# Kernel tuning notes

Measured on AMD Instinct MI355X. Metric: run time of the kernel, lower is better.

The kernel has to match this reference:

```python
import jax, jax.numpy as jnp
import numpy as np

NUM_NODES = 100000
NUM_EDGES = 1600000
NUM_GRAPHS = 512
HIDDEN = 128
LAYERS = 3
NUM_CLASSES = 10
BN_EPS = 1e-5


def setup_inputs() -> dict:
    key = jax.random.key(0)
    ks = jax.random.split(key, 12)
    x = jax.random.normal(ks[0], (NUM_NODES, HIDDEN), dtype=jnp.float32)
    edge_index = jax.random.randint(ks[1], (2, NUM_EDGES), 0, NUM_NODES, dtype=jnp.int32)
    batch = jnp.sort(jax.random.randint(ks[2], (NUM_NODES,), 0, NUM_GRAPHS, dtype=jnp.int32))
    s = 1.0 / np.sqrt(HIDDEN)
    W1 = jax.random.normal(ks[3], (LAYERS, HIDDEN, HIDDEN), dtype=jnp.float32) * s
    b1 = jnp.zeros((LAYERS, HIDDEN), dtype=jnp.float32)
    W2 = jax.random.normal(ks[4], (LAYERS, HIDDEN, HIDDEN), dtype=jnp.float32) * s
    b2 = jnp.zeros((LAYERS, HIDDEN), dtype=jnp.float32)
    gamma = jnp.ones((LAYERS, HIDDEN), dtype=jnp.float32)
    beta = jnp.zeros((LAYERS, HIDDEN), dtype=jnp.float32)
    eps_gin = jnp.zeros((LAYERS,), dtype=jnp.float32)  # train_eps init 0
    lin1_w = jax.random.normal(ks[5], (LAYERS * HIDDEN, HIDDEN), dtype=jnp.float32) * (1.0 / np.sqrt(LAYERS * HIDDEN))
    lin1_b = jnp.zeros((HIDDEN,), dtype=jnp.float32)
    lin2_w = jax.random.normal(ks[6], (HIDDEN, NUM_CLASSES), dtype=jnp.float32) * s
    lin2_b = jnp.zeros((NUM_CLASSES,), dtype=jnp.float32)
    return {"x": x, "edge_index": edge_index, "batch": batch,
            "W1": W1, "b1": b1, "W2": W2, "b2": b2,
            "gamma": gamma, "beta": beta, "eps_gin": eps_gin,
            "lin1_w": lin1_w, "lin1_b": lin1_b, "lin2_w": lin2_w, "lin2_b": lin2_b}


def _batchnorm(h, g, b):
    mu = jnp.mean(h, axis=0, keepdims=True)
    var = jnp.var(h, axis=0, keepdims=True)
    return (h - mu) * jax.lax.rsqrt(var + BN_EPS) * g + b


def reference(x, edge_index, batch, W1, b1, W2, b2, gamma, beta, eps_gin,
              lin1_w, lin1_b, lin2_w, lin2_b):
    src, dst = edge_index[0], edge_index[1]
    n = x.shape[0]
    h = x
    layer_hs = []
    for l in range(LAYERS):
        # scatter-add neighbor aggregation: agg[i] = sum_{j->i} h[j]
        agg = jax.ops.segment_sum(h[src], dst, num_segments=n)
        z = (1.0 + eps_gin[l]) * h + agg
        z = jax.nn.relu(z @ W1[l] + b1[l])
        z = jax.nn.relu(z @ W2[l] + b2[l])
        h = _batchnorm(z, gamma[l], beta[l])
        layer_hs.append(h)
    h_cat = jnp.concatenate(layer_hs, axis=-1)  # [N, LAYERS*HIDDEN]
    # global mean pool per graph
    sums = jax.ops.segment_sum(h_cat, batch, num_segments=NUM_GRAPHS)
    counts = jax.ops.segment_sum(jnp.ones((n, 1), h_cat.dtype), batch, num_segments=NUM_GRAPHS)
    g = sums / jnp.maximum(counts, 1.0)
    g = jax.nn.relu(g @ lin1_w + lin1_b)
    # dropout is identity in inference
    return g @ lin2_w + lin2_b
```

## Files before the change

### kernel.cpp

```cpp
#include <hip/hip_runtime.h>

#define HID 128
#define NGRAPH 512
#define NLAYERS 3
#define BN_EPS 1e-5f
#define NPB 256
#define EB 4096

typedef __attribute__((ext_vector_type(8))) short bf16x8;
typedef __attribute__((ext_vector_type(4))) float f32x4;
typedef __attribute__((ext_vector_type(2))) float f32x2;

__device__ inline unsigned short f2bf(float x) {
    union { float f; unsigned u; } v; v.f = x;
    unsigned r = v.u + 0x7FFFu + ((v.u >> 16) & 1u);
    return (unsigned short)(r >> 16);
}
__device__ inline float bf2f(unsigned short b) {
    union { float f; unsigned u; } v; v.u = ((unsigned)b) << 16; return v.f;
}
__device__ inline f32x2 bfp(unsigned u) {
    union { unsigned q; float f; } lo, hi;
    lo.q = u << 16; hi.q = u & 0xFFFF0000u;
    f32x2 r; r[0] = lo.f; r[1] = hi.f; return r;
}

__global__ void k_prep(float* __restrict__ stats, float* __restrict__ gsum,
                       const float4* __restrict__ x4, ushort* __restrict__ xb, int total4,
                       const float* __restrict__ W1, ushort* __restrict__ w1h, ushort* __restrict__ w1l,
                       const float* __restrict__ W2, ushort* __restrict__ w2h, ushort* __restrict__ w2l,
                       int wtotal, int xblocks,
                       const int* __restrict__ dst, int E, int* __restrict__ blkcnt) {
    __shared__ int hist[512];
    int b = blockIdx.x, t = threadIdx.x;
    if (b < 768) {
        if (b == 0) for (int l = 0; l < NLAYERS; ++l) stats[l * 256 + t] = 0.0f;
        gsum[b * 256 + t] = 0.0f;
    } else if (b < 1152) {
        int gid = (b - 768) * 256 + t;
        const float* W; ushort *Wh, *Wl; int e;
        if (gid < wtotal) { W = W1; Wh = w1h; Wl = w1l; e = gid; }
        else              { W = W2; Wh = w2h; Wl = w2l; e = gid - wtotal; }
        if (e < wtotal) {
            int l = e >> 14, rem = e & 16383, k = rem >> 7, n = rem & 127;
            float v = W[e];
            ushort hi = f2bf(v);
            ushort lo = f2bf(v - bf2f(hi));
            int o = (l << 14) + (n << 7) + k;
            Wh[o] = hi; Wl[o] = lo;
        }
    } else if (b < 1152 + xblocks) {
        int i = (b - 1152) * 256 + t;
        if (i < total4) {
            float4 v = x4[i];
            uint2 p;
            p.x = ((unsigned)f2bf(v.y) << 16) | f2bf(v.x);
            p.y = ((unsigned)f2bf(v.w) << 16) | f2bf(v.z);
            ((uint2*)xb)[i] = p;
        }
    } else {
        int b2 = b - (1152 + xblocks);
        hist[t] = 0; hist[t + 256] = 0;
        __syncthreads();
        int base = b2 * EB;
        #pragma unroll
        for (int i = 0; i < 16; ++i) {
            int e = base + i * 256 + t;
            if (e < E) atomicAdd(&hist[dst[e] >> 8], 1);
        }
        __syncthreads();
        blkcnt[b2 * 512 + t]       = hist[t];
        blkcnt[b2 * 512 + t + 256] = hist[t + 256];
    }
}

__global__ __launch_bounds__(256) void k_btot_reduce(const int* __restrict__ blkcnt,
                                                     int eblk, int* __restrict__ tot) {
    __shared__ int sh[256];
    int b = blockIdx.x;
    int t = threadIdx.x;
    int s = 0;
    for (int j = t; j < eblk; j += 256) s += blkcnt[j * 512 + b];
    sh[t] = s;
    __syncthreads();
    #pragma unroll
    for (int k = 128; k > 0; k >>= 1) {
        if (t < k) sh[t] += sh[t + k];
        __syncthreads();
    }
    if (t == 0) tot[b] = sh[0];
}

__global__ __launch_bounds__(512) void k_bscan(const int* __restrict__ tot, int nb, int E,
                                               int* __restrict__ bbase, int* __restrict__ rowptrN) {
    __shared__ int sh[512];
    int t = threadIdx.x;
    sh[t] = (t < nb) ? tot[t] : 0;
    __syncthreads();
    #pragma unroll
    for (int s = 1; s < 512; s <<= 1) {
        int v = (t >= s) ? sh[t - s] : 0;
        __syncthreads();
        sh[t] += v;
        __syncthreads();
    }
    if (t < nb) bbase[t] = (t == 0) ? 0 : sh[t - 1];
    if (t == 0) { bbase[nb] = E; *rowptrN = E; }
}

__global__ __launch_bounds__(512) void k_colscan(int* __restrict__ blkcnt, int eblk,
                                                 const int* __restrict__ bbase) {
    __shared__ int sh[512];
    int t = threadIdx.x;
    int b = blockIdx.x;
    sh[t] = (t < eblk) ? blkcnt[t * 512 + b] : 0;
    __syncthreads();
    #pragma unroll
    for (int s = 1; s < 512; s <<= 1) {
        int v = (t >= s) ? sh[t - s] : 0;
        __syncthreads();
        sh[t] += v;
        __syncthreads();
    }
    int excl = (t == 0) ? 0 : sh[t - 1];
    if (t < eblk) blkcnt[t * 512 + b] = bbase[b] + excl;
}

__global__ __launch_bounds__(256) void k_bscatter(const int* __restrict__ src,
                                                  const int* __restrict__ dst, int E,
                                                  const int* __restrict__ blkcnt,
                                                  unsigned* __restrict__ pairs) {
    __shared__ int hist[512];
    __shared__ int lbase[512];
    int t = threadIdx.x;
    hist[t] = 0; hist[t + 256] = 0;
    lbase[t]       = blkcnt[blockIdx.x * 512 + t];
    lbase[t + 256] = blkcnt[blockIdx.x * 512 + t + 256];
    __syncthreads();
    int base = blockIdx.x * EB;
    #pragma unroll
    for (int i = 0; i < 16; ++i) {
        int e = base + i * 256 + t;
        if (e < E) {
            int d = dst[e];
            int b = d >> 8;
            int pos = lbase[b] + atomicAdd(&hist[b], 1);
            pairs[pos] = ((unsigned)(d & 255) << 24) | (unsigned)src[e];
        }
    }
}

__global__ __launch_bounds__(256) void k_bbuild(const unsigned* __restrict__ pairs,
                                                const int* __restrict__ bbase, int N,
                                                int* __restrict__ rowptr, int* __restrict__ csr) {
    __shared__ int cnt[256];
    __shared__ int off[256];
    int t = threadIdx.x;
    int b = blockIdx.x;
    int base = bbase[b], bcount = bbase[b + 1] - base;
    cnt[t] = 0;
    __syncthreads();
    for (int i = t; i < bcount; i += 256) atomicAdd(&cnt[pairs[base + i] >> 24], 1);
    __syncthreads();
    off[t] = cnt[t];
    __syncthreads();
    for (int s = 1; s < 256; s <<= 1) {
        int v = (t >= s) ? off[t - s] : 0;
        __syncthreads();
        off[t] += v;
        __syncthreads();
    }
    int excl = (t == 0) ? 0 : off[t - 1];
    int node = b * NPB + t;
    if (node < N) rowptr[node] = base + excl;
    cnt[t] = excl;
    __syncthreads();
    for (int i = t; i < bcount; i += 256) {
        unsigned p = pairs[base + i];
        int dl = p >> 24;
        int pos = base + atomicAdd(&cnt[dl], 1);
        csr[pos] = (int)(p & 0xFFFFFFu);
    }
}

__global__ __launch_bounds__(256, 6) void k_agg(
        const int* __restrict__ rowptr, const int* __restrict__ csr_src,
        const uint2* __restrict__ hinb,
        const float* __restrict__ prev_stats,
        const float* __restrict__ g_row, const float* __restrict__ be_row,
        const float* __restrict__ eps_gin, int layer,
        ushort* __restrict__ z0out, int N) {
    const int t = threadIdx.x;
    const int lane = t & 63;
    const int wv = t >> 6;
    const int q = lane >> 4;
    const int f = lane & 15;

    f32x2 scv2[4], shv2[4];
    if (prev_stats) {
        float invn = 1.0f / (float)N;
        #pragma unroll
        for (int d = 0; d < 4; ++d) {
            #pragma unroll
            for (int h = 0; h < 2; ++h) {
                int fi = f * 8 + d * 2 + h;
                float mu = prev_stats[fi] * invn;
                float var = prev_stats[128 + fi] * invn - mu * mu;
                float inv = rsqrtf(var + BN_EPS);
                float scj = g_row[fi] * inv;
                scv2[d][h] = scj; shv2[d][h] = be_row[fi] - mu * scj;
            }
        }
    } else {
        #pragma unroll
        for (int d = 0; d < 4; ++d) { scv2[d] = (f32x2){1.f, 1.f}; shv2[d] = (f32x2){0.f, 0.f}; }
    }
    float e1 = 1.0f + eps_gin[layer];
    const uint4* hin4 = (const uint4*)hinb;

    int r = blockIdx.x * 16 + wv * 4 + q;
    f32x2 a2[4];
    #pragma unroll
    for (int d = 0; d < 4; ++d) a2[d] = (f32x2){0.f, 0.f};
    float cdeg = 0.f;
    if (r < N) {
        int beg = rowptr[r], end = rowptr[r + 1];
        uint4 hv = hin4[(size_t)r * 16 + f];
        a2[0] = e1 * bfp(hv.x); a2[1] = e1 * bfp(hv.y);
        a2[2] = e1 * bfp(hv.z); a2[3] = e1 * bfp(hv.w);
        int p = beg;
        for (; p + 8 <= end; p += 8) {
            int s0 = csr_src[p],     s1 = csr_src[p + 1], s2 = csr_src[p + 2], s3 = csr_src[p + 3];
            int s4 = csr_src[p + 4], s5 = csr_src[p + 5], s6 = csr_src[p + 6], s7 = csr_src[p + 7];
            uint4 v0 = hin4[(size_t)s0 * 16 + f];
            uint4 v1 = hin4[(size_t)s1 * 16 + f];
            uint4 v2 = hin4[(size_t)s2 * 16 + f];
            uint4 v3 = hin4[(size_t)s3 * 16 + f];
            uint4 v4 = hin4[(size_t)s4 * 16 + f];
            uint4 v5 = hin4[(size_t)s5 * 16 + f];
            uint4 v6 = hin4[(size_t)s6 * 16 + f];
            uint4 v7 = hin4[(size_t)s7 * 16 + f];
            a2[0] += ((bfp(v0.x) + bfp(v1.x)) + (bfp(v2.x) + bfp(v3.x)))
                   + ((bfp(v4.x) + bfp(v5.x)) + (bfp(v6.x) + bfp(v7.x)));
            a2[1] += ((bfp(v0.y) + bfp(v1.y)) + (bfp(v2.y) + bfp(v3.y)))
                   + ((bfp(v4.y) + bfp(v5.y)) + (bfp(v6.y) + bfp(v7.y)));
            a2[2] += ((bfp(v0.z) + bfp(v1.z)) + (bfp(v2.z) + bfp(v3.z)))
                   + ((bfp(v4.z) + bfp(v5.z)) + (bfp(v6.z) + bfp(v7.z)));
            a2[3] += ((bfp(v0.w) + bfp(v1.w)) + (bfp(v2.w) + bfp(v3.w)))
                   + ((bfp(v4.w) + bfp(v5.w)) + (bfp(v6.w) + bfp(v7.w)));
        }
        if (p < end) {
            int last = end - 1;
            int c1 = min(p + 1, last), c2 = min(p + 2, last), c3 = min(p + 3, last);
            int c4 = min(p + 4, last), c5 = min(p + 5, last), c6 = min(p + 6, last);
            int s0 = csr_src[p],  s1 = csr_src[c1], s2 = csr_src[c2], s3 = csr_src[c3];
            int s4 = csr_src[c4], s5 = csr_src[c5], s6 = csr_src[c6];
            uint4 v0 = hin4[(size_t)s0 * 16 + f];
            uint4 v1 = hin4[(size_t)s1 * 16 + f];
            uint4 v2 = hin4[(size_t)s2 * 16 + f];
            uint4 v3 = hin4[(size_t)s3 * 16 + f];
            uint4 v4 = hin4[(size_t)s4 * 16 + f];
            uint4 v5 = hin4[(size_t)s5 * 16 + f];
            uint4 v6 = hin4[(size_t)s6 * 16 + f];
            int rem = end - p;
            unsigned m1 = (rem > 1) ? 0xFFFFFFFFu : 0u;
            unsigned m2 = (rem > 2) ? 0xFFFFFFFFu : 0u;
            unsigned m3 = (rem > 3) ? 0xFFFFFFFFu : 0u;
            unsigned m4 = (rem > 4) ? 0xFFFFFFFFu : 0u;
            unsigned m5 = (rem > 5) ? 0xFFFFFFFFu : 0u;
            unsigned m6 = (rem > 6) ? 0xFFFFFFFFu : 0u;
            a2[0] += ((bfp(v0.x) + bfp(v1.x & m1)) + (bfp(v2.x & m2) + bfp(v3.x & m3)))
                   + ((bfp(v4.x & m4) + bfp(v5.x & m5)) + bfp(v6.x & m6));
            a2[1] += ((bfp(v0.y) + bfp(v1.y & m1)) + (bfp(v2.y & m2) + bfp(v3.y & m3)))
                   + ((bfp(v4.y & m4) + bfp(v5.y & m5)) + bfp(v6.y & m6));
            a2[2] += ((bfp(v0.z) + bfp(v1.z & m1)) + (bfp(v2.z & m2) + bfp(v3.z & m3)))
                   + ((bfp(v4.z & m4) + bfp(v5.z & m5)) + bfp(v6.z & m6));
            a2[3] += ((bfp(v0.w) + bfp(v1.w & m1)) + (bfp(v2.w & m2) + bfp(v3.w & m3)))
                   + ((bfp(v4.w & m4) + bfp(v5.w & m5)) + bfp(v6.w & m6));
        }
        cdeg = e1 + (float)(end - beg);
    }
    f32x2 rr2[4];
    #pragma unroll
    for (int d = 0; d < 4; ++d) rr2[d] = scv2[d] * a2[d] + cdeg * shv2[d];
    uint4 ph;
    ph.x = ((unsigned)f2bf(rr2[0][1]) << 16) | f2bf(rr2[0][0]);
    ph.y = ((unsigned)f2bf(rr2[1][1]) << 16) | f2bf(rr2[1][0]);
    ph.z = ((unsigned)f2bf(rr2[2][1]) << 16) | f2bf(rr2[2][0]);
    ph.w = ((unsigned)f2bf(rr2[3][1]) << 16) | f2bf(rr2[3][0]);
    if (r < N) ((uint4*)z0out)[(size_t)r * 16 + f] = ph;
}

__global__ __launch_bounds__(256, 4) void k_mlp_dense(
        const uint4* __restrict__ z0, int layer, const int* __restrict__ batch,
        const ushort* __restrict__ w1h, const ushort* __restrict__ w1l,
        const float* __restrict__ b1,
        const ushort* __restrict__ w2h, const ushort* __restrict__ w2l,
        const float* __restrict__ b2,
        ushort* __restrict__ Hout, float* __restrict__ stat_sum, float* __restrict__ stat_sq,
        float* __restrict__ gsum, int N) {
    __shared__ __align__(16) ushort smem[8192];
    const int t = threadIdx.x;
    const int lane = t & 63;
    const int wv = t >> 6;
    const int li = lane & 15;
    const int kq = lane >> 4;
    const int n0 = wv * 32;
    const int row0 = blockIdx.x * 64;
    const int swz = (li & 7) * 4;

    {
        const uint4 zz = {0u, 0u, 0u, 0u};
        #pragma unroll
        for (int i = 0; i < 4; ++i) {
            int idx = i * 256 + t;
            int r = idx >> 4, f = idx & 15;
            uint4 v = (row0 + r < N) ? z0[(size_t)(row0 + r) * 16 + f] : zz;
            ((uint4*)smem)[r * 16 + (f ^ (r & 7))] = v;
        }
    }
    __syncthreads();

    f32x4 acc[4][2];
    #pragma unroll
    for (int i = 0; i < 4; ++i) {
        acc[i][0] = (f32x4){0.f, 0.f, 0.f, 0.f};
        acc[i][1] = (f32x4){0.f, 0.f, 0.f, 0.f};
    }

    #pragma unroll
    for (int ch = 0; ch < 2; ++ch) {
        #pragma unroll
        for (int ks = 0; ks < 2; ++ks) {
            int kcol = ch * 8 + ks * 4 + kq;
            bf16x8 bh[2], bl[2];
            #pragma unroll
            for (int nt = 0; nt < 2; ++nt) {
                size_t wo = (size_t)(n0 + nt * 16 + li) * 128 + (ch * 64 + ks * 32 + kq * 8);
                bh[nt] = *(const bf16x8*)&w1h[wo];
                bl[nt] = *(const bf16x8*)&w1l[wo];
            }
            #pragma unroll
            for (int mt = 0; mt < 4; ++mt) {
                int r = mt * 16 + li;
                int hw = (r * 16 + (kcol ^ (li & 7))) * 8;
                bf16x8 ah = *(const bf16x8*)&smem[hw];
                #pragma unroll
                for (int nt = 0; nt < 2; ++nt) {
                    acc[mt][nt] = __builtin_amdgcn_mfma_f32_16x16x32_bf16(ah, bh[nt], acc[mt][nt], 0, 0, 0);
                    acc[mt][nt] = __builtin_amdgcn_mfma_f32_16x16x32_bf16(ah, bl[nt], acc[mt][nt], 0, 0, 0);
                }
            }
        }
    }

    float bz0 = b1[n0 + li], bz1 = b1[n0 + 16 + li];
    __syncthreads();
    #pragma unroll
    for (int mt = 0; mt < 4; ++mt) {
        #pragma unroll
        for (int nt = 0; nt < 2; ++nt) {
            int c = n0 + nt * 16 + li;
            int dk = c >> 1;
            int halfbase = (dk >> 5) * 32;
            int dlow = dk & 31;
            int codd = c & 1;
            float bias = nt ? bz1 : bz0;
            #pragma unroll
            for (int reg = 0; reg < 4; ++reg) {
                int r = mt * 16 + kq * 4 + reg;
                float v = fmaxf(acc[mt][nt][reg] + bias, 0.f);
                int us = (r * 64 + halfbase + (dlow ^ ((r & 7) * 4))) * 2 + codd;
                smem[us] = f2bf(v);
            }
        }
    }
    #pragma unroll
    for (int i = 0; i < 4; ++i) {
        acc[i][0] = (f32x4){0.f, 0.f, 0.f, 0.f};
        acc[i][1] = (f32x4){0.f, 0.f, 0.f, 0.f};
    }
    __syncthreads();

    #pragma unroll
    for (int ch = 0; ch < 2; ++ch) {
        #pragma unroll
        for (int ks = 0; ks < 2; ++ks) {
            bf16x8 bh[2], bl[2];
            #pragma unroll
            for (int nt = 0; nt < 2; ++nt) {
                size_t wo = (size_t)(n0 + nt * 16 + li) * 128 + (ch * 64 + ks * 32 + kq * 8);
                bh[nt] = *(const bf16x8*)&w2h[wo];
                bl[nt] = *(const bf16x8*)&w2l[wo];
            }
            int aoff = (ks * 16 + kq * 4) ^ swz;
            #pragma unroll
            for (int mt = 0; mt < 4; ++mt) {
                int idx = ((mt * 16 + li) * 64 + ch * 32 + aoff) * 2;
                bf16x8 ah = *(const bf16x8*)&smem[idx];
                #pragma unroll
                for (int nt = 0; nt < 2; ++nt) {
                    acc[mt][nt] = __builtin_amdgcn_mfma_f32_16x16x32_bf16(ah, bh[nt], acc[mt][nt], 0, 0, 0);
                    acc[mt][nt] = __builtin_amdgcn_mfma_f32_16x16x32_bf16(ah, bl[nt], acc[mt][nt], 0, 0, 0);
                }
            }
        }
    }

    float bb0 = b2[n0 + li], bb1 = b2[n0 + 16 + li];
    int btr[4][4];
    #pragma unroll
    for (int mt = 0; mt < 4; ++mt)
        #pragma unroll
        for (int reg = 0; reg < 4; ++reg) {
            int grow = row0 + mt * 16 + kq * 4 + reg;
            btr[mt][reg] = (grow < N) ? batch[grow] : -1;
        }
    __syncthreads();
    float s0 = 0.f, q0 = 0.f, s1 = 0.f, q1 = 0.f;
    #pragma unroll
    for (int mt = 0; mt < 4; ++mt) {
        #pragma unroll
        for (int reg = 0; reg < 4; ++reg) {
            int r = mt * 16 + kq * 4 + reg;
            float v0 = fmaxf(acc[mt][0][reg] + bb0, 0.f);
            float v1 = fmaxf(acc[mt][1][reg] + bb1, 0.f);
            smem[r * 128 + n0 + li]      = f2bf(v0);
            smem[r * 128 + n0 + 16 + li] = f2bf(v1);
            if (btr[mt][reg] >= 0) {
                s0 += v0; q0 += v0 * v0; s1 += v1; q1 += v1 * v1;
            }
        }
    }
    __syncthreads();
    {
        int valid = N - row0; if (valid > 64) valid = 64;
        int tot = valid * 16;
        for (int i = t; i < tot; i += 256) {
            int r = i >> 4, c = i & 15;
            ((uint4*)&Hout[(size_t)(row0 + r) * HID])[c] = ((const uint4*)smem)[r * 16 + c];
        }
    }
    s0 += __shfl_xor(s0, 16); s0 += __shfl_xor(s0, 32);
    q0 += __shfl_xor(q0, 16); q0 += __shfl_xor(q0, 32);
    s1 += __shfl_xor(s1, 16); s1 += __shfl_xor(s1, 32);
    q1 += __shfl_xor(q1, 16); q1 += __shfl_xor(q1, 32);
    if (kq == 0) {
        unsafeAtomicAdd(&stat_sum[n0 + li], s0);
        unsafeAtomicAdd(&stat_sq[n0 + li], q0);
        unsafeAtomicAdd(&stat_sum[n0 + 16 + li], s1);
        unsafeAtomicAdd(&stat_sq[n0 + 16 + li], q1);
    }
    int lastr = N - 1; if (lastr > row0 + 63) lastr = row0 + 63;
    int g_lo = batch[row0], g_hi = batch[lastr];
    int loff = layer * HID;
    for (int g = g_lo; g <= g_hi; ++g) {
        float p0 = 0.f, p1 = 0.f;
        #pragma unroll
        for (int mt = 0; mt < 4; ++mt)
            #pragma unroll
            for (int reg = 0; reg < 4; ++reg) {
                if (btr[mt][reg] == g) {
                    p0 += fmaxf(acc[mt][0][reg] + bb0, 0.f);
                    p1 += fmaxf(acc[mt][1][reg] + bb1, 0.f);
                }
            }
        p0 += __shfl_xor(p0, 16); p0 += __shfl_xor(p0, 32);
        p1 += __shfl_xor(p1, 16); p1 += __shfl_xor(p1, 32);
        if (kq == 0) {
            unsafeAtomicAdd(&gsum[(size_t)g * 384 + loff + n0 + li], p0);
            unsafeAtomicAdd(&gsum[(size_t)g * 384 + loff + n0 + 16 + li], p1);
        }
    }
}

__global__ __launch_bounds__(128) void k_mlp(const int* __restrict__ batch, int N,
                     const float* __restrict__ gsum, const float* __restrict__ stats,
                     const float* __restrict__ gamma, const float* __restrict__ beta,
                     const float* __restrict__ w1, const float* __restrict__ b1,
                     const float* __restrict__ w2, const float* __restrict__ b2,
                     float* __restrict__ out) {
    __shared__ float gl[384];
    __shared__ float hh[128];
    int g = blockIdx.x, t = threadIdx.x;
    int start, end;
    { int lo = 0, hi = N; while (lo < hi) { int m = (lo + hi) >> 1; if (batch[m] < g) lo = m + 1; else hi = m; } start = lo; }
    { int lo = start, hi = N; while (lo < hi) { int m = (lo + hi) >> 1; if (batch[m] < g + 1) lo = m + 1; else hi = m; } end = lo; }
    float cnt = (float)(end - start);
    float invc = 1.0f / fmaxf(cnt, 1.0f);
    float invn = 1.0f / (float)N;
    #pragma unroll
    for (int l = 0; l < NLAYERS; ++l) {
        float mu = stats[l * 256 + t] * invn;
        float var = stats[l * 256 + 128 + t] * invn - mu * mu;
        float inv = rsqrtf(var + BN_EPS);
        float sc = gamma[l * HID + t] * inv;
        float sh = beta[l * HID + t] - mu * sc;
        gl[l * 128 + t] = (gsum[(size_t)g * 384 + l * 128 + t] * sc + sh * cnt) * invc;
    }
    __syncthreads();
    float acc = b1[t];
    for (int k = 0; k < 384; ++k) acc = fmaf(gl[k], w1[k * HID + t], acc);
    hh[t] = fmaxf(acc, 0.f);
    __syncthreads();
    if (t < 10) {
        float a2 = b2[t];
        for (int k = 0; k < 128; ++k) a2 = fmaf(hh[k], w2[k * 10 + t], a2);
        out[g * 10 + t] = a2;
    }
}

extern "C" void kernel_launch(void* const* d_in, const int* in_sizes, int n_in,
                              void* d_out, int out_size, void* d_ws, size_t ws_size,
                              hipStream_t stream) {
    const float* x     = (const float*)d_in[0];
    const int*   ei    = (const int*)d_in[1];
    const int*   batch = (const int*)d_in[2];
    const float* W1    = (const float*)d_in[3];
    const float* b1    = (const float*)d_in[4];
    const float* W2    = (const float*)d_in[5];
    const float* b2    = (const float*)d_in[6];
    const float* gamma = (const float*)d_in[7];
    const float* beta  = (const float*)d_in[8];
    const float* epsg  = (const float*)d_in[9];
    const float* l1w   = (const float*)d_in[10];
    const float* l1b   = (const float*)d_in[11];
    const float* l2w   = (const float*)d_in[12];
    const float* l2b   = (const float*)d_in[13];

    const int N = in_sizes[0] / HID;
    const int E = in_sizes[1] / 2;
    const int* src = ei;
    const int* dst = ei + E;
    const int nb = (N + NPB - 1) / NPB;
    const int eblk = (E + EB - 1) / EB;

    float* w = (float*)d_ws;
    const size_t NF = (size_t)N * HID;
    ushort* xb    = (ushort*)(w + NF);
    ushort* hb[3] = { xb + NF, xb + 2 * NF, xb + 3 * NF };
    ushort* z0buf = xb + 4 * NF;
    float* stats  = w + 4 * NF;
    float* gsum   = stats + 768;
    int*   rowptr = (int*)(gsum + (size_t)NGRAPH * 384);
    int*   csr    = rowptr + N + 1;
    int*   bbase  = csr + E;
    int*   btot   = bbase + nb + 2;
    ushort* wt  = (ushort*)(((uintptr_t)(btot + nb + 1) + 15) & ~(uintptr_t)15);
    ushort* w1h = wt;
    ushort* w1l = wt + 49152;
    ushort* w2h = wt + 98304;
    ushort* w2l = wt + 147456;

    unsigned* pairs  = (unsigned*)w;
    int*      blkcnt = (int*)(w + 2 * 1024 * 1024);

    const int total4 = (int)(NF / 4);
    const int xblocks = (total4 + 255) / 256;
    const int prep_blocks = 1152 + xblocks + eblk;
    k_prep<<<prep_blocks, 256, 0, stream>>>(stats, gsum, (const float4*)x, xb, total4,
                                            W1, w1h, w1l, W2, w2h, w2l, NLAYERS * HID * HID,
                                            xblocks, dst, E, blkcnt);

    k_btot_reduce<<<nb, 256, 0, stream>>>(blkcnt, eblk, btot);
    k_bscan<<<1, 512, 0, stream>>>(btot, nb, E, bbase, rowptr + N);
    k_colscan<<<nb, 512, 0, stream>>>(blkcnt, eblk, bbase);
    k_bscatter<<<eblk, 256, 0, stream>>>(src, dst, E, blkcnt, pairs);
    k_bbuild<<<nb, 256, 0, stream>>>(pairs, bbase, N, rowptr, csr);

    for (int l = 0; l < NLAYERS; ++l) {
        const ushort* hin = (l == 0) ? xb : hb[l - 1];
        const float* pstats = (l == 0) ? nullptr : (stats + (l - 1) * 256);
        const float* grow_  = gamma + (l == 0 ? 0 : (l - 1)) * HID;
        const float* brow_  = beta  + (l == 0 ? 0 : (l - 1)) * HID;

        k_agg<<<(N + 15) / 16, 256, 0, stream>>>(
            rowptr, csr, (const uint2*)hin, pstats, grow_, brow_, epsg, l, z0buf, N);

        k_mlp_dense<<<(N + 63) / 64, 256, 0, stream>>>(
            (const uint4*)z0buf, l, batch,
            w1h + (size_t)l * 16384, w1l + (size_t)l * 16384, b1 + l * HID,
            w2h + (size_t)l * 16384, w2l + (size_t)l * 16384, b2 + l * HID,
            hb[l], stats + l * 256, stats + l * 256 + 128, gsum, N);
    }

    k_mlp<<<NGRAPH, 128, 0, stream>>>(batch, N, gsum, stats, gamma, beta,
                                      l1w, l1b, l2w, l2b, (float*)d_out);
}
```

Baseline: 566.9 us.

## Preload MLP weights into registers and shard BN stat atomics across slices

The dense MLP kernel now loads all W1/W2 hi/lo bf16 fragments into registers once at kernel start instead of inside the k-loops. It relaxes launch bounds from 4 to 2 blocks per SM to make room for the extra registers. BatchNorm sum and sum-of-squares atomics are spread across 8 slices keyed by block index to cut atomic contention, and a small fold kernel per layer reduces them into the stats buffer. The cost is lower occupancy, higher register pressure and three extra tiny kernel launches.

```diff
diff --git a/kernel.cpp b/kernel.cpp
--- a/kernel.cpp
+++ b/kernel.cpp
@@ -25,7 +25,7 @@
     f32x2 r; r[0] = lo.f; r[1] = hi.f; return r;
 }
 
-__global__ void k_prep(float* __restrict__ stats, float* __restrict__ gsum,
+__global__ void k_prep(float* __restrict__ ssliced, float* __restrict__ gsum,
                        const float4* __restrict__ x4, ushort* __restrict__ xb, int total4,
                        const float* __restrict__ W1, ushort* __restrict__ w1h, ushort* __restrict__ w1l,
                        const float* __restrict__ W2, ushort* __restrict__ w2h, ushort* __restrict__ w2l,
@@ -34,7 +34,7 @@
     __shared__ int hist[512];
     int b = blockIdx.x, t = threadIdx.x;
     if (b < 768) {
-        if (b == 0) for (int l = 0; l < NLAYERS; ++l) stats[l * 256 + t] = 0.0f;
+        if (b < 24) ssliced[b * 256 + t] = 0.0f;
         gsum[b * 256 + t] = 0.0f;
     } else if (b < 1152) {
         int gid = (b - 768) * 256 + t;
@@ -291,13 +291,13 @@
     if (r < N) ((uint4*)z0out)[(size_t)r * 16 + f] = ph;
 }
 
-__global__ __launch_bounds__(256, 4) void k_mlp_dense(
+__global__ __launch_bounds__(256, 2) void k_mlp_dense(
         const uint4* __restrict__ z0, int layer, const int* __restrict__ batch,
         const ushort* __restrict__ w1h, const ushort* __restrict__ w1l,
         const float* __restrict__ b1,
         const ushort* __restrict__ w2h, const ushort* __restrict__ w2l,
         const float* __restrict__ b2,
-        ushort* __restrict__ Hout, float* __restrict__ stat_sum, float* __restrict__ stat_sq,
+        ushort* __restrict__ Hout, float* __restrict__ stat_sl,
         float* __restrict__ gsum, int N) {
     __shared__ __align__(16) ushort smem[8192];
     const int t = threadIdx.x;
@@ -309,6 +309,21 @@
     const int row0 = blockIdx.x * 64;
     const int swz = (li & 7) * 4;
 
+    bf16x8 w1hr[8], w1lr[8], w2hr[8], w2lr[8];
+    #pragma unroll
+    for (int ch = 0; ch < 2; ++ch)
+        #pragma unroll
+        for (int ks = 0; ks < 2; ++ks)
+            #pragma unroll
+            for (int nt = 0; nt < 2; ++nt) {
+                int i = ch * 4 + ks * 2 + nt;
+                size_t wo = (size_t)(n0 + nt * 16 + li) * 128 + (ch * 64 + ks * 32 + kq * 8);
+                w1hr[i] = *(const bf16x8*)&w1h[wo];
+                w1lr[i] = *(const bf16x8*)&w1l[wo];
+                w2hr[i] = *(const bf16x8*)&w2h[wo];
+                w2lr[i] = *(const bf16x8*)&w2l[wo];
+            }
+
     {
         const uint4 zz = {0u, 0u, 0u, 0u};
         #pragma unroll
@@ -333,13 +348,6 @@
         #pragma unroll
         for (int ks = 0; ks < 2; ++ks) {
             int kcol = ch * 8 + ks * 4 + kq;
-            bf16x8 bh[2], bl[2];
-            #pragma unroll
-            for (int nt = 0; nt < 2; ++nt) {
-                size_t wo = (size_t)(n0 + nt * 16 + li) * 128 + (ch * 64 + ks * 32 + kq * 8);
-                bh[nt] = *(const bf16x8*)&w1h[wo];
-                bl[nt] = *(const bf16x8*)&w1l[wo];
-            }
             #pragma unroll
             for (int mt = 0; mt < 4; ++mt) {
                 int r = mt * 16 + li;
@@ -347,8 +355,9 @@
                 bf16x8 ah = *(const bf16x8*)&smem[hw];
                 #pragma unroll
                 for (int nt = 0; nt < 2; ++nt) {
-                    acc[mt][nt] = __builtin_amdgcn_mfma_f32_16x16x32_bf16(ah, bh[nt], acc[mt][nt], 0, 0, 0);
-                    acc[mt][nt] = __builtin_amdgcn_mfma_f32_16x16x32_bf16(ah, bl[nt], acc[mt][nt], 0, 0, 0);
+                    int i = ch * 4 + ks * 2 + nt;
+                    acc[mt][nt] = __builtin_amdgcn_mfma_f32_16x16x32_bf16(ah, w1hr[i], acc[mt][nt], 0, 0, 0);
+                    acc[mt][nt] = __builtin_amdgcn_mfma_f32_16x16x32_bf16(ah, w1lr[i], acc[mt][nt], 0, 0, 0);
                 }
             }
         }
@@ -386,13 +395,6 @@
     for (int ch = 0; ch < 2; ++ch) {
         #pragma unroll
         for (int ks = 0; ks < 2; ++ks) {
-            bf16x8 bh[2], bl[2];
-            #pragma unroll
-            for (int nt = 0; nt < 2; ++nt) {
-                size_t wo = (size_t)(n0 + nt * 16 + li) * 128 + (ch * 64 + ks * 32 + kq * 8);
-                bh[nt] = *(const bf16x8*)&w2h[wo];
-                bl[nt] = *(const bf16x8*)&w2l[wo];
-            }
             int aoff = (ks * 16 + kq * 4) ^ swz;
             #pragma unroll
             for (int mt = 0; mt < 4; ++mt) {
@@ -400,8 +402,9 @@
                 bf16x8 ah = *(const bf16x8*)&smem[idx];
                 #pragma unroll
                 for (int nt = 0; nt < 2; ++nt) {
-                    acc[mt][nt] = __builtin_amdgcn_mfma_f32_16x16x32_bf16(ah, bh[nt], acc[mt][nt], 0, 0, 0);
-                    acc[mt][nt] = __builtin_amdgcn_mfma_f32_16x16x32_bf16(ah, bl[nt], acc[mt][nt], 0, 0, 0);
+                    int i = ch * 4 + ks * 2 + nt;
+                    acc[mt][nt] = __builtin_amdgcn_mfma_f32_16x16x32_bf16(ah, w2hr[i], acc[mt][nt], 0, 0, 0);
+                    acc[mt][nt] = __builtin_amdgcn_mfma_f32_16x16x32_bf16(ah, w2lr[i], acc[mt][nt], 0, 0, 0);
                 }
             }
         }
@@ -446,10 +449,11 @@
     s1 += __shfl_xor(s1, 16); s1 += __shfl_xor(s1, 32);
     q1 += __shfl_xor(q1, 16); q1 += __shfl_xor(q1, 32);
     if (kq == 0) {
-        unsafeAtomicAdd(&stat_sum[n0 + li], s0);
-        unsafeAtomicAdd(&stat_sq[n0 + li], q0);
-        unsafeAtomicAdd(&stat_sum[n0 + 16 + li], s1);
-        unsafeAtomicAdd(&stat_sq[n0 + 16 + li], q1);
+        float* ss = stat_sl + (blockIdx.x & 7) * 768;
+        unsafeAtomicAdd(&ss[n0 + li], s0);
+        unsafeAtomicAdd(&ss[128 + n0 + li], q0);
+        unsafeAtomicAdd(&ss[n0 + 16 + li], s1);
+        unsafeAtomicAdd(&ss[128 + n0 + 16 + li], q1);
     }
     int lastr = N - 1; if (lastr > row0 + 63) lastr = row0 + 63;
     int g_lo = batch[row0], g_hi = batch[lastr];
@@ -472,6 +476,15 @@
             unsafeAtomicAdd(&gsum[(size_t)g * 384 + loff + n0 + 16 + li], p1);
         }
     }
+}
+
+__global__ __launch_bounds__(256) void k_sfold(const float* __restrict__ sliced,
+                                               float* __restrict__ out) {
+    int t = threadIdx.x;
+    float s = 0.f;
+    #pragma unroll
+    for (int k = 0; k < 8; ++k) s += sliced[k * 768 + t];
+    out[t] = s;
 }
 
 __global__ __launch_bounds__(128) void k_mlp(const int* __restrict__ batch, int N,
@@ -541,7 +554,8 @@
     ushort* hb[3] = { xb + NF, xb + 2 * NF, xb + 3 * NF };
     ushort* z0buf = xb + 4 * NF;
     float* stats  = w + 4 * NF;
-    float* gsum   = stats + 768;
+    float* sliced = stats + 768;
+    float* gsum   = sliced + 6144;
     int*   rowptr = (int*)(gsum + (size_t)NGRAPH * 384);
     int*   csr    = rowptr + N + 1;
     int*   bbase  = csr + E;
@@ -558,7 +572,7 @@
     const int total4 = (int)(NF / 4);
     const int xblocks = (total4 + 255) / 256;
     const int prep_blocks = 1152 + xblocks + eblk;
-    k_prep<<<prep_blocks, 256, 0, stream>>>(stats, gsum, (const float4*)x, xb, total4,
+    k_prep<<<prep_blocks, 256, 0, stream>>>(sliced, gsum, (const float4*)x, xb, total4,
                                             W1, w1h, w1l, W2, w2h, w2l, NLAYERS * HID * HID,
                                             xblocks, dst, E, blkcnt);
 
@@ -581,7 +595,9 @@
             (const uint4*)z0buf, l, batch,
             w1h + (size_t)l * 16384, w1l + (size_t)l * 16384, b1 + l * HID,
             w2h + (size_t)l * 16384, w2l + (size_t)l * 16384, b2 + l * HID,
-            hb[l], stats + l * 256, stats + l * 256 + 128, gsum, N);
+            hb[l], sliced + l * 256, gsum, N);
+
+        k_sfold<<<1, 256, 0, stream>>>(sliced + l * 256, stats + l * 256);
     }
 
     k_mlp<<<NGRAPH, 128, 0, stream>>>(batch, N, gsum, stats, gamma, beta,
```

Measured after the change: 524.0 us. 7.6% less time.
